# Kernel optimization log

Hardware: AMD Instinct MI355X
Metric: run time of the kernel (lower is better)

Reference implementation:

```python
import jax, jax.numpy as jnp
import numpy as np

LAYERS = 10
EPS = 1e-08


def setup_inputs() -> dict:
    key = jax.random.key(0)
    # [B, agents, N, N] assignment logits; row 0 along dim 2 is the depot row
    output = jax.random.normal(key, (32, 8, 512, 512), dtype=jnp.float32)
    return {"output": output}


def reference(output):
    # Max-subtraction for numerical stability before exp.
    # Depot row: max over dim 3 only. Other rows: max over dims (1, 3).
    if LAYERS > 0:
        depots_max = jnp.max(output[:, :, :1, :], axis=3, keepdims=True)
        others_max = jnp.max(output[:, :, 1:, :], axis=(1, 3), keepdims=True)
        output = jnp.concatenate(
            [output[:, :, :1, :] - depots_max,
             output[:, :, 1:, :] - others_max],
            axis=2,
        )
    output = jnp.exp(output)
    # Sinkhorn-style alternating normalization; transpose(2,3) each iter
    # alternates which axis gets normalized.
    for _ in range(LAYERS):
        output = jnp.maximum(output, EPS)
        starts = output[:, :, :1, :]
        starts = starts / jnp.sum(starts, axis=3, keepdims=True)
        nexts = output[:, :, 1:, :]
        nexts = nexts / jnp.sum(nexts, axis=(1, 3), keepdims=True)
        output = jnp.concatenate([starts, nexts], axis=2)
        output = jnp.swapaxes(output, 2, 3)
    if LAYERS % 2 != 0:
        output = jnp.swapaxes(output, 2, 3)
    return output
```

## Files before the change

### kernel.cpp

```cpp
#include <hip/hip_runtime.h>
#include <hip/hip_cooperative_groups.h>
#include <math.h>

#define B 32
#define H 8
#define N 512
#define NBLK 256
#define TPB 512
#define RPB 64
#define OFF_E0   8388608
#define OFF_EC   (OFF_E0 + 131072)
#define OFF_PA   (OFF_EC + 131072)
#define OFF_PB   (OFF_PA + 131072)
#define OFF_C0A  (OFF_PB + 131072)
#define OFF_C0B  (OFF_C0A + 2048)

typedef float f32x4 __attribute__((ext_vector_type(4)));

__device__ __forceinline__ float atomLoad(const float* p) {
    return __hip_atomic_load(p, __ATOMIC_RELAXED, __HIP_MEMORY_SCOPE_AGENT);
}
__device__ __forceinline__ void atomStore(float* p, float v) {
    __hip_atomic_store(p, v, __ATOMIC_RELAXED, __HIP_MEMORY_SCOPE_AGENT);
}

__device__ __forceinline__ void group_barrier(int* cnt, int target) {
    __syncthreads();
    if (threadIdx.x == 0) {
        __hip_atomic_fetch_add(cnt, 1, __ATOMIC_RELAXED, __HIP_MEMORY_SCOPE_AGENT);
        while (__hip_atomic_load(cnt, __ATOMIC_RELAXED, __HIP_MEMORY_SCOPE_AGENT) < target)
            __builtin_amdgcn_s_sleep(2);
    }
    __syncthreads();
}

__global__ __launch_bounds__(128) void k_build(const float* __restrict__ in,
                                               float* __restrict__ G,
                                               float* __restrict__ E0,
                                               float* __restrict__ Ec) {
    const int i = blockIdx.x;
    const int b = blockIdx.y;
    const int t = threadIdx.x;
    const size_t inb = (size_t)b * H * N * N;
    float4 acc = make_float4(0.f, 0.f, 0.f, 0.f);
#pragma unroll
    for (int h = 0; h < H; ++h) {
        const float4 x = *reinterpret_cast<const float4*>(
            in + inb + ((size_t)h * N + i) * N + t * 4);
        float4 e;
        e.x = __expf(x.x); e.y = __expf(x.y); e.z = __expf(x.z); e.w = __expf(x.w);
        acc.x += e.x; acc.y += e.y; acc.z += e.z; acc.w += e.w;
        if (t == 0) Ec[(b * H + h) * N + i] = e.x;
        if (i == 0) *reinterpret_cast<float4*>(E0 + (b * H + h) * N + t * 4) = e;
    }
    *reinterpret_cast<float4*>(G + ((size_t)b * N + i) * N + t * 4) = acc;
}

__global__ __launch_bounds__(TPB) void k_coop(const float* __restrict__ G,
                                              const float* __restrict__ E0,
                                              const float* __restrict__ Ec,
                                              float* __restrict__ partA,
                                              float* __restrict__ partB,
                                              float* __restrict__ c0pA,
                                              float* __restrict__ c0pB,
                                              float* __restrict__ rv,
                                              float* __restrict__ r0v,
                                              float* __restrict__ cv,
                                              float* __restrict__ c0v,
                                              int* __restrict__ counters) {
    __shared__ float Gs[RPB][N];
    __shared__ float E0g[N];
    __shared__ float vec[N];
    __shared__ float EcS[H][RPB];
    __shared__ float rloc[RPB];
    __shared__ float c0rec[H];
    __shared__ float r0loc_s;

    const int blk = blockIdx.x;
    const int b = blk >> 3;
    const int g = blk & 7;
    const int rbase = g * RPB;
    const bool owner = (g == 0);
    const int tid = threadIdx.x;
    const int w = tid >> 6, lane = tid & 63;
    int* cnt = counters + b * 16;

    {
        const float4* Gg = reinterpret_cast<const float4*>(G + ((size_t)(b * N) + rbase) * N);
        float4* Gl = reinterpret_cast<float4*>(&Gs[0][0]);
#pragma unroll
        for (int k = 0; k < RPB * N / 4 / TPB; ++k) {
            const int t = k * TPB + tid;
            __builtin_amdgcn_global_load_lds(
                (const __attribute__((address_space(1))) void*)(Gg + t),
                (__attribute__((address_space(3))) void*)(Gl + t),
                16, 0, 0);
        }
    }
    for (int t = tid; t < H * RPB; t += TPB)
        EcS[t / RPB][t % RPB] = Ec[(b * H + (t / RPB)) * N + rbase + (t % RPB)];
    E0g[tid] = E0[(b * H + g) * N + tid];
    const float E00g = Ec[(b * H + g) * N];
    __syncthreads();

    for (int it = 0; it < 5; ++it) {
        if (it == 0) {
            vec[tid] = (tid == 0) ? 0.0f : 1.0f;
            if (tid < H) c0rec[tid] = 1.0f;
        } else {
            const float* pr = (it & 1) ? partB : partA;
            pr += (size_t)b * 8 * N;
            float cs = 0.0f;
#pragma unroll
            for (int gg = 0; gg < 8; ++gg) cs += atomLoad(&pr[gg * N + tid]);
            vec[tid] = (tid == 0) ? 0.0f : 1.0f / cs;
            if (tid < H) {
                const float* qr = (it & 1) ? c0pB : c0pA;
                qr += b * 8 * H;
                float s = 0.0f;
#pragma unroll
                for (int gg = 0; gg < 8; ++gg) s += atomLoad(&qr[gg * H + tid]);
                c0rec[tid] = 1.0f / s;
            }
        }
        __syncthreads();
        float cj[8];
#pragma unroll
        for (int k = 0; k < 8; ++k) cj[k] = vec[lane + 64 * k];
#pragma unroll
        for (int r8 = 0; r8 < 8; ++r8) {
            const int il = w * 8 + r8;
            float pacc = 0.0f;
#pragma unroll
            for (int k = 0; k < 8; ++k) pacc += Gs[il][lane + 64 * k] * cj[k];
#pragma unroll
            for (int s = 32; s > 0; s >>= 1) pacc += __shfl_down(pacc, s, 64);
            if (lane == 0) {
                float s2 = pacc;
#pragma unroll
                for (int h = 0; h < H; ++h) s2 += EcS[h][il] * c0rec[h];
                float rva = 1.0f / s2;
                rloc[il] = rva;
                if (it == 4) rv[b * N + rbase + il] = rva;
            }
        }
        if (w == g) {
            float pacc = 0.0f;
#pragma unroll
            for (int k = 0; k < 8; ++k) pacc += E0g[lane + 64 * k] * cj[k];
#pragma unroll
            for (int s = 32; s > 0; s >>= 1) pacc += __shfl_down(pacc, s, 64);
            if (lane == 0) {
                float v = 1.0f / (pacc + E00g * c0rec[g]);
                r0loc_s = v;
                if (it == 4) r0v[b * H + g] = v;
            }
        }
        __syncthreads();
        {
            float* pw = ((it + 1) & 1) ? partB : partA;
            float* qw = ((it + 1) & 1) ? c0pB : c0pA;
            const float r0l = r0loc_s;
            float acc = 0.0f;
            const int il0 = owner ? 1 : 0;
#pragma unroll 8
            for (int il = il0; il < RPB; ++il) acc += Gs[il][tid] * rloc[il];
            acc += E0g[tid] * r0l;
            atomStore(&pw[((size_t)(b * 8) + g) * N + tid], acc);
            float q = EcS[w][lane] * ((owner && lane == 0) ? 0.0f : rloc[lane]);
            if (w == g && lane == 0) q += E00g * r0l;
#pragma unroll
            for (int s = 32; s > 0; s >>= 1) q += __shfl_down(q, s, 64);
            if (lane == 0) atomStore(&qw[(b * 8 + g) * H + w], q);
        }
        group_barrier(cnt, (it + 1) * 8);
    }
    if (owner) {
        const float* pr = partB + (size_t)b * 8 * N;
        float cs = 0.0f;
#pragma unroll
        for (int gg = 0; gg < 8; ++gg) cs += atomLoad(&pr[gg * N + tid]);
        cv[b * N + tid] = (tid == 0) ? 1.0f : 1.0f / cs;
        if (tid < H) {
            const float* qr = c0pB + b * 8 * H;
            float s = 0.0f;
#pragma unroll
            for (int gg = 0; gg < 8; ++gg) s += atomLoad(&qr[gg * H + tid]);
            c0v[b * H + tid] = 1.0f / s;
        }
    }
}

__global__ __launch_bounds__(256) void k_final(const float* __restrict__ in,
                                               const float* __restrict__ rv,
                                               const float* __restrict__ r0v,
                                               const float* __restrict__ cv,
                                               const float* __restrict__ c0v,
                                               float* __restrict__ out) {
    const size_t v0 = (size_t)blockIdx.x * 1024 + threadIdx.x;
#pragma unroll
    for (int s = 0; s < 4; ++s) {
        const size_t v = v0 + (size_t)s * 256;
        const int j4 = (int)(v & 127);
        size_t rest = v >> 7;
        const int i = (int)(rest & 511); rest >>= 9;
        const int h = (int)(rest & 7);
        const int b = (int)(rest >> 3);
        const float R = (i == 0) ? r0v[b * H + h] : rv[b * N + i];
        const f32x4 x = __builtin_nontemporal_load(reinterpret_cast<const f32x4*>(in) + v);
        float4 cl = reinterpret_cast<const float4*>(cv + b * N)[j4];
        if (j4 == 0) cl.x = c0v[b * H + h];
        f32x4 o;
        o.x = __expf(x.x) * R * cl.x;
        o.y = __expf(x.y) * R * cl.y;
        o.z = __expf(x.z) * R * cl.z;
        o.w = __expf(x.w) * R * cl.w;
        __builtin_nontemporal_store(o, reinterpret_cast<f32x4*>(out) + v);
    }
}

extern "C" void kernel_launch(void* const* d_in, const int* in_sizes, int n_in,
                              void* d_out, int out_size, void* d_ws, size_t ws_size,
                              hipStream_t stream) {
    (void)in_sizes; (void)n_in; (void)out_size; (void)ws_size;
    const float* in = (const float*)d_in[0];
    float* out = (float*)d_out;
    float* ws = (float*)d_ws;

    float* rv  = ws;
    float* cv  = ws + 16384;
    float* r0v = ws + 32768;
    float* c0v = ws + 33024;
    int* counters = (int*)(ws + 33280);

    float* G   = out;
    float* E0  = out + OFF_E0;
    float* Ec  = out + OFF_EC;
    float* pA  = out + OFF_PA;
    float* pB  = out + OFF_PB;
    float* c0A = out + OFF_C0A;
    float* c0B = out + OFF_C0B;

    hipMemsetAsync(counters, 0, B * 16 * sizeof(int), stream);

    k_build<<<dim3(N, B), 128, 0, stream>>>(in, G, E0, Ec);

    void* args[] = {(void*)&G, (void*)&E0, (void*)&Ec, (void*)&pA, (void*)&pB,
                    (void*)&c0A, (void*)&c0B, (void*)&rv, (void*)&r0v,
                    (void*)&cv, (void*)&c0v, (void*)&counters};
    hipLaunchCooperativeKernel(reinterpret_cast<void*>(k_coop), dim3(NBLK), dim3(TPB),
                               args, 0, stream);

    k_final<<<16384, 256, 0, stream>>>(in, rv, r0v, cv, c0v, out);
}
```

Measured before the change: 211.8 us.

## Fold counter reset into build kernel, transpose partial-sum layout, batch final loads

Removes the separate hipMemsetAsync by zeroing the barrier counters inside k_build. Transposes the partial column-sum buffers so each thread reads its 8 group partials contiguously with 64-bit atomic loads. Shortens the barrier spin sleep. k_final now issues 8 nontemporal loads per thread up front before computing, with half as many blocks, to raise memory-level parallelism at the cost of more registers.

After: 206.1 us. 2.7% less time.

```diff
diff --git a/kernel.cpp b/kernel.cpp
--- a/kernel.cpp
+++ b/kernel.cpp
@@ -20,6 +20,13 @@
 __device__ __forceinline__ float atomLoad(const float* p) {
     return __hip_atomic_load(p, __ATOMIC_RELAXED, __HIP_MEMORY_SCOPE_AGENT);
 }
+__device__ __forceinline__ float2 atomLoad2(const float* p) {
+    unsigned long long u = __hip_atomic_load(
+        reinterpret_cast<const unsigned long long*>(p),
+        __ATOMIC_RELAXED, __HIP_MEMORY_SCOPE_AGENT);
+    union { unsigned long long u; float2 f; } cvt; cvt.u = u;
+    return cvt.f;
+}
 __device__ __forceinline__ void atomStore(float* p, float v) {
     __hip_atomic_store(p, v, __ATOMIC_RELAXED, __HIP_MEMORY_SCOPE_AGENT);
 }
@@ -29,7 +36,7 @@
     if (threadIdx.x == 0) {
         __hip_atomic_fetch_add(cnt, 1, __ATOMIC_RELAXED, __HIP_MEMORY_SCOPE_AGENT);
         while (__hip_atomic_load(cnt, __ATOMIC_RELAXED, __HIP_MEMORY_SCOPE_AGENT) < target)
-            __builtin_amdgcn_s_sleep(2);
+            __builtin_amdgcn_s_sleep(1);
     }
     __syncthreads();
 }
@@ -37,10 +44,15 @@
 __global__ __launch_bounds__(128) void k_build(const float* __restrict__ in,
                                                float* __restrict__ G,
                                                float* __restrict__ E0,
-                                               float* __restrict__ Ec) {
+                                               float* __restrict__ Ec,
+                                               int* __restrict__ counters) {
     const int i = blockIdx.x;
     const int b = blockIdx.y;
     const int t = threadIdx.x;
+    if (i == 0 && b == 0) {
+#pragma unroll
+        for (int k = 0; k < 4; ++k) counters[k * 128 + t] = 0;
+    }
     const size_t inb = (size_t)b * H * N * N;
     float4 acc = make_float4(0.f, 0.f, 0.f, 0.f);
 #pragma unroll
@@ -97,8 +109,7 @@
                 16, 0, 0);
         }
     }
-    for (int t = tid; t < H * RPB; t += TPB)
-        EcS[t / RPB][t % RPB] = Ec[(b * H + (t / RPB)) * N + rbase + (t % RPB)];
+    EcS[tid >> 6][tid & 63] = Ec[(b * H + (tid >> 6)) * N + rbase + (tid & 63)];
     E0g[tid] = E0[(b * H + g) * N + tid];
     const float E00g = Ec[(b * H + g) * N];
     __syncthreads();
@@ -109,17 +120,23 @@
             if (tid < H) c0rec[tid] = 1.0f;
         } else {
             const float* pr = (it & 1) ? partB : partA;
-            pr += (size_t)b * 8 * N;
+            pr += ((size_t)b * N + tid) * 8;
             float cs = 0.0f;
 #pragma unroll
-            for (int gg = 0; gg < 8; ++gg) cs += atomLoad(&pr[gg * N + tid]);
+            for (int k = 0; k < 4; ++k) {
+                float2 d = atomLoad2(pr + 2 * k);
+                cs += d.x + d.y;
+            }
             vec[tid] = (tid == 0) ? 0.0f : 1.0f / cs;
             if (tid < H) {
                 const float* qr = (it & 1) ? c0pB : c0pA;
-                qr += b * 8 * H;
+                qr += (b * 8 + tid) * 8;
                 float s = 0.0f;
 #pragma unroll
-                for (int gg = 0; gg < 8; ++gg) s += atomLoad(&qr[gg * H + tid]);
+                for (int k = 0; k < 4; ++k) {
+                    float2 d = atomLoad2(qr + 2 * k);
+                    s += d.x + d.y;
+                }
                 c0rec[tid] = 1.0f / s;
             }
         }
@@ -166,26 +183,32 @@
 #pragma unroll 8
             for (int il = il0; il < RPB; ++il) acc += Gs[il][tid] * rloc[il];
             acc += E0g[tid] * r0l;
-            atomStore(&pw[((size_t)(b * 8) + g) * N + tid], acc);
+            atomStore(&pw[((size_t)b * N + tid) * 8 + g], acc);
             float q = EcS[w][lane] * ((owner && lane == 0) ? 0.0f : rloc[lane]);
             if (w == g && lane == 0) q += E00g * r0l;
 #pragma unroll
             for (int s = 32; s > 0; s >>= 1) q += __shfl_down(q, s, 64);
-            if (lane == 0) atomStore(&qw[(b * 8 + g) * H + w], q);
+            if (lane == 0) atomStore(&qw[(b * 8 + w) * 8 + g], q);
         }
         group_barrier(cnt, (it + 1) * 8);
     }
     if (owner) {
-        const float* pr = partB + (size_t)b * 8 * N;
+        const float* pr = partB + ((size_t)b * N + tid) * 8;
         float cs = 0.0f;
 #pragma unroll
-        for (int gg = 0; gg < 8; ++gg) cs += atomLoad(&pr[gg * N + tid]);
+        for (int k = 0; k < 4; ++k) {
+            float2 d = atomLoad2(pr + 2 * k);
+            cs += d.x + d.y;
+        }
         cv[b * N + tid] = (tid == 0) ? 1.0f : 1.0f / cs;
         if (tid < H) {
-            const float* qr = c0pB + b * 8 * H;
+            const float* qr = c0pB + (b * 8 + tid) * 8;
             float s = 0.0f;
 #pragma unroll
-            for (int gg = 0; gg < 8; ++gg) s += atomLoad(&qr[gg * H + tid]);
+            for (int k = 0; k < 4; ++k) {
+                float2 d = atomLoad2(qr + 2 * k);
+                s += d.x + d.y;
+            }
             c0v[b * H + tid] = 1.0f / s;
         }
     }
@@ -197,9 +220,13 @@
                                                const float* __restrict__ cv,
                                                const float* __restrict__ c0v,
                                                float* __restrict__ out) {
-    const size_t v0 = (size_t)blockIdx.x * 1024 + threadIdx.x;
-#pragma unroll
-    for (int s = 0; s < 4; ++s) {
+    const size_t v0 = (size_t)blockIdx.x * 2048 + threadIdx.x;
+    f32x4 x[8];
+#pragma unroll
+    for (int s = 0; s < 8; ++s)
+        x[s] = __builtin_nontemporal_load(reinterpret_cast<const f32x4*>(in) + v0 + (size_t)s * 256);
+#pragma unroll
+    for (int s = 0; s < 8; ++s) {
         const size_t v = v0 + (size_t)s * 256;
         const int j4 = (int)(v & 127);
         size_t rest = v >> 7;
@@ -207,14 +234,13 @@
         const int h = (int)(rest & 7);
         const int b = (int)(rest >> 3);
         const float R = (i == 0) ? r0v[b * H + h] : rv[b * N + i];
-        const f32x4 x = __builtin_nontemporal_load(reinterpret_cast<const f32x4*>(in) + v);
         float4 cl = reinterpret_cast<const float4*>(cv + b * N)[j4];
         if (j4 == 0) cl.x = c0v[b * H + h];
         f32x4 o;
-        o.x = __expf(x.x) * R * cl.x;
-        o.y = __expf(x.y) * R * cl.y;
-        o.z = __expf(x.z) * R * cl.z;
-        o.w = __expf(x.w) * R * cl.w;
+        o.x = __expf(x[s].x) * R * cl.x;
+        o.y = __expf(x[s].y) * R * cl.y;
+        o.z = __expf(x[s].z) * R * cl.z;
+        o.w = __expf(x[s].w) * R * cl.w;
         __builtin_nontemporal_store(o, reinterpret_cast<f32x4*>(out) + v);
     }
 }
@@ -241,9 +267,7 @@
     float* c0A = out + OFF_C0A;
     float* c0B = out + OFF_C0B;
 
-    hipMemsetAsync(counters, 0, B * 16 * sizeof(int), stream);
-
-    k_build<<<dim3(N, B), 128, 0, stream>>>(in, G, E0, Ec);
+    k_build<<<dim3(N, B), 128, 0, stream>>>(in, G, E0, Ec, counters);
 
     void* args[] = {(void*)&G, (void*)&E0, (void*)&Ec, (void*)&pA, (void*)&pB,
                     (void*)&c0A, (void*)&c0B, (void*)&rv, (void*)&r0v,
@@ -251,5 +275,5 @@
     hipLaunchCooperativeKernel(reinterpret_cast<void*>(k_coop), dim3(NBLK), dim3(TPB),
                                args, 0, stream);
 
-    k_final<<<16384, 256, 0, stream>>>(in, rv, r0v, cv, c0v, out);
-}
+    k_final<<<8192, 256, 0, stream>>>(in, rv, r0v, cv, c0v, out);
+}
```
